# Performance work log

Hardware: AMD Instinct MI355X
Metric: run time of the kernel (lower is better)

## Reference

```python
import jax, jax.numpy as jnp
import numpy as np

BATCH, D_MODEL, D_STATE, L = 16, 512, 64, 4096
DT_MIN, DT_MAX = 1e-3, 0.1


def setup_inputs() -> dict:
    key = jax.random.key(0)
    ks = jax.random.split(key, 8)
    u = jax.random.normal(ks[0], (BATCH, D_MODEL, L), jnp.float32)
    # S4DKernel params (faithful init)
    log_dt = (jax.random.uniform(ks[1], (D_MODEL,), jnp.float32)
              * (np.log(DT_MAX) - np.log(DT_MIN)) + np.log(DT_MIN)).astype(jnp.float32)
    log_A_real = jnp.log(0.5 * jnp.ones((D_MODEL, D_STATE), jnp.float32))
    A_imag = jnp.pi * jnp.tile(jnp.arange(D_STATE, dtype=jnp.float32), (D_MODEL, 1))
    B_re = jnp.ones((D_MODEL, D_STATE), jnp.float32)
    B_im = jnp.zeros((D_MODEL, D_STATE), jnp.float32)
    # torch.randn(cfloat): re/im each N(0, 1/2)
    C_re = (2.0 ** -0.5) * jax.random.normal(ks[2], (D_MODEL, D_STATE), jnp.float32)
    C_im = (2.0 ** -0.5) * jax.random.normal(ks[3], (D_MODEL, D_STATE), jnp.float32)
    D = jax.random.normal(ks[4], (D_MODEL,), jnp.float32)
    # Conv1d(d_model, 2*d_model, k=1) weight squeezed to (2d, d)
    W_out = jax.random.normal(ks[5], (2 * D_MODEL, D_MODEL), jnp.float32) / np.sqrt(D_MODEL)
    b_out = jnp.zeros((2 * D_MODEL,), jnp.float32)
    # decoder Linear(d_model, 1)
    W_dec = jax.random.normal(ks[6], (1, D_MODEL), jnp.float32) / np.sqrt(D_MODEL)
    b_dec = jnp.zeros((1,), jnp.float32)
    return dict(u=u, log_dt=log_dt, log_A_real=log_A_real, A_imag=A_imag,
                B_re=B_re, B_im=B_im, C_re=C_re, C_im=C_im, D=D,
                W_out=W_out, b_out=b_out, W_dec=W_dec, b_dec=b_dec)


def _s4d_kernel(log_dt, log_A_real, A_imag, B_re, B_im, C_re, C_im, length):
    # ZOH discretization of diagonal SSM -> real conv kernel (d_model, length)
    dt = jnp.exp(log_dt)                                  # (d,)
    A = -jnp.exp(log_A_real) + 1j * A_imag                # (d, n)
    dtA = A * dt[:, None]                                 # (d, n)
    A_bar = jnp.exp(dtA)
    B = B_re + 1j * B_im
    C = C_re + 1j * C_im
    B_bar = (A_bar - 1.0) / A * B                         # (d, n)
    t = jnp.arange(length)
    # A_bar ** t == exp(dtA * t): (d, n, length) complex Vandermonde
    vand = jnp.exp(dtA[:, :, None] * t)
    K = jnp.einsum('dn,dnl->dl', C * B_bar, vand)         # sum over states
    return K.real


def reference(u, log_dt, log_A_real, A_imag, B_re, B_im, C_re, C_im, D,
              W_out, b_out, W_dec, b_dec):
    length = u.shape[-1]
    d_model = u.shape[1]
    K = _s4d_kernel(log_dt, log_A_real, A_imag, B_re, B_im, C_re, C_im, length)
    # depthwise causal conv: torch conv1d(padding=L-1, groups=d)[..., :L]
    y = jax.lax.conv_general_dilated(
        u, K[:, None, :], window_strides=(1,), padding=[(length - 1, 0)],
        feature_group_count=d_model, dimension_numbers=('NCH', 'OIH', 'NCH'))
    y = y + u * D[:, None]
    y = jax.nn.gelu(y, approximate=False)                 # exact GELU (erf)
    # 1x1 conv: d -> 2d
    y = jnp.einsum('oc,bcl->bol', W_out, y) + b_out[None, :, None]
    a, g = jnp.split(y, 2, axis=-2)                       # GLU on channel dim
    y = a * jax.nn.sigmoid(g)
    pooled = y.mean(axis=-1)                              # (B, d)
    return pooled @ W_dec.T + b_dec                       # (B, 1)
```

## Files before the change

### kernel.cpp

```cpp
#include <hip/hip_runtime.h>


#define UOFF_POOLED 1048576
#define UOFF_WBF    1081344
#define UOFF_UBF    2129920
#define UOFF_YRAW   69238784
#define UOFF_SEEDB  136347648
#define UOFF_KBUF   153124864

typedef __attribute__((ext_vector_type(8))) short short8;
typedef __attribute__((ext_vector_type(4))) float f32x4;
typedef __attribute__((ext_vector_type(2))) float f2;
typedef unsigned short ushort_t;
typedef unsigned int uint_t;

__device__ __forceinline__ ushort_t f2bf(float f) {
  uint_t u = __float_as_uint(f);
  u = (u + 0x7FFF + ((u >> 16) & 1)) >> 16;
  return (ushort_t)u;
}
__device__ __forceinline__ float bf2f(ushort_t v) {
  return __uint_as_float(((uint_t)v) << 16);
}

__device__ __forceinline__ void gload16(const ushort_t* g, ushort_t* l) {
  __builtin_amdgcn_global_load_lds(
      (const __attribute__((address_space(1))) void*)g,
      (__attribute__((address_space(3))) void*)l, 16, 0, 0);
}

__device__ __forceinline__ f2 cexp(float dr, float di, float t) {
  float e = expf(dr * t);
  float ph = di * t;
  return (f2){e * cosf(ph), e * sinf(ph)};
}

__global__ __launch_bounds__(256) void k_prep(
    const float* __restrict__ u, ushort_t* __restrict__ u_bf,
    const float* __restrict__ W_out, ushort_t* __restrict__ wbf,
    const float* __restrict__ log_dt, const float* __restrict__ log_A_real,
    const float* __restrict__ A_imag,
    const float* __restrict__ B_re, const float* __restrict__ B_im,
    const float* __restrict__ C_re, const float* __restrict__ C_im,
    float* __restrict__ p_ar, float* __restrict__ p_ai,
    float* __restrict__ p_wr, float* __restrict__ p_wi,
    float* __restrict__ p_dr, float* __restrict__ p_di,
    float* __restrict__ p_lr, float* __restrict__ p_li) {
  int bid = blockIdx.x;
  if (bid < 16384) {
    size_t i = (size_t)bid * 256 + threadIdx.x;
    const float4* p = (const float4*)u + 2 * i;
    float4 a = p[0], b = p[1];
    uint4 v;
    v.x = (uint_t)f2bf(a.x) | ((uint_t)f2bf(a.y) << 16);
    v.y = (uint_t)f2bf(a.z) | ((uint_t)f2bf(a.w) << 16);
    v.z = (uint_t)f2bf(b.x) | ((uint_t)f2bf(b.y) << 16);
    v.w = (uint_t)f2bf(b.z) | ((uint_t)f2bf(b.w) << 16);
    ((uint4*)u_bf)[i] = v;
  } else if (bid < 16384 + 2048) {
    int i = (bid - 16384) * 256 + threadIdx.x;
    if (i < 1024 * 512) wbf[i] = f2bf(W_out[i]);
  } else {
    int i = (bid - 18432) * 256 + threadIdx.x;
    int d = i >> 6;
    float dt  = expf(log_dt[d]);
    float Are = -expf(log_A_real[i]);
    float Aim = A_imag[i];
    float dre = dt * Are, dim = dt * Aim;
    float em  = expf(dre);
    float abr = em * cosf(dim);
    float abi = em * sinf(dim);
    float nr = abr - 1.0f, ni = abi;
    float inv = 1.0f / (Are * Are + Aim * Aim);
    float br = (nr * Are + ni * Aim) * inv;
    float bi = (ni * Are - nr * Aim) * inv;
    float Br = B_re[i], Bi = B_im[i];
    float b2r = br * Br - bi * Bi;
    float b2i = br * Bi + bi * Br;
    float Cr = C_re[i], Ci = C_im[i];
    p_ar[i] = abr; p_ai[i] = abi;
    p_wr[i] = Cr * b2r - Ci * b2i;
    p_wi[i] = Cr * b2i + Ci * b2r;
    p_dr[i] = dre; p_di[i] = dim;
    float eL = expf(dre * 4096.0f);
    float phL = dim * 4096.0f;
    p_lr[i] = eL * cosf(phL);
    p_li[i] = eL * sinf(phL);
  }
}

__global__ __launch_bounds__(256) void k_hk(
    const ushort_t* __restrict__ u_bf,
    const float* __restrict__ p_ar, const float* __restrict__ p_ai,
    const float* __restrict__ p_wr, const float* __restrict__ p_wi,
    const float* __restrict__ p_dr, const float* __restrict__ p_di,
    const float* __restrict__ Dvec,
    float2* __restrict__ Hbuf, ushort_t* __restrict__ Kbuf) {
  __shared__ ushort_t VLD[2][128][128];
  int bid = blockIdx.x;
  int d = bid >> 1;
  int tid = threadIdx.x;

  if (bid & 1) {
    int lane = tid & 63;
    int x0 = (tid >> 6) * 128;
    int i = d * 64 + lane;
    float ar = p_ar[i], ai = p_ai[i];
    float wr = p_wr[i], wi = p_wi[i];
    float Dd = Dvec[d];
    f2 e = cexp(p_dr[i], p_di[i], (float)(3584 + x0));
    float zr = wr * e.x - wi * e.y;
    float zi = wr * e.y + wi * e.x;
    for (int bb = 0; bb < 8; ++bb) {
      float s[16];
#pragma unroll
      for (int j = 0; j < 16; ++j) {
        s[j] = zr;
        float tr = zr * ar - zi * ai;
        zi = zr * ai + zi * ar;
        zr = tr;
      }
      float out = 0.f;
#pragma unroll
      for (int j = 0; j < 16; ++j) {
        float r = s[j];
#pragma unroll
        for (int off = 1; off < 64; off <<= 1) r += __shfl_xor(r, off, 64);
        if (lane == j) out = r;
      }
      if (lane < 16) {
        int x = x0 + bb * 16 + lane;
        Kbuf[d * 512 + x] = f2bf(x == 511 ? out + Dd : out);
      }
    }
    return;
  }

  int wv = tid >> 6, lane = tid & 63;
  int wm = wv >> 1, wn = wv & 1;
  int lrow = lane & 15, quad = lane >> 4;

  int m = tid & 127, chalf = tid >> 7;
  int nn = m >> 1, pp = m & 1;
  float ar = p_ar[d * 64 + nn], ai = p_ai[d * 64 + nn];
  float dr = p_dr[d * 64 + nn], di = p_di[d * 64 + nn];

  f32x4 acc[4][4];
#pragma unroll
  for (int mt = 0; mt < 4; ++mt)
#pragma unroll
    for (int nt = 0; nt < 4; ++nt) acc[mt][nt] = (f32x4){0.f, 0.f, 0.f, 0.f};

  auto gen = [&](int kt, int bs) {
    f2 z = cexp(dr, di, (float)(kt * 128 + chalf * 64));
#pragma unroll
    for (int g8 = 0; g8 < 8; ++g8) {
      ushort_t vals[8];
#pragma unroll
      for (int e = 0; e < 8; ++e) {
        vals[e] = f2bf(pp ? z.y : z.x);
        float zr = z.x * ar - z.y * ai;
        z.y = z.x * ai + z.y * ar;
        z.x = zr;
      }
      int g = (chalf * 64 + g8 * 8) >> 3;
      int gph = g ^ (m & 7);
      uint4 pk;
      pk.x = (uint_t)vals[0] | ((uint_t)vals[1] << 16);
      pk.y = (uint_t)vals[2] | ((uint_t)vals[3] << 16);
      pk.z = (uint_t)vals[4] | ((uint_t)vals[5] << 16);
      pk.w = (uint_t)vals[6] | ((uint_t)vals[7] << 16);
      *(uint4*)&VLD[bs][m][gph << 3] = pk;
    }
  };

  gen(0, 0);
  __syncthreads();
  for (int kt = 0; kt < 4; ++kt) {
    int cur = kt & 1;
    if (kt < 3) gen(kt + 1, cur ^ 1);
#pragma unroll
    for (int kb = 0; kb < 4; ++kb) {
      int kbase = kb * 32 + quad * 8;
      short8 af[4], bf[4];
#pragma unroll
      for (int mt = 0; mt < 4; ++mt) {
        int mrow = wm * 64 + mt * 16 + lrow;
        int gph = (kbase >> 3) ^ (mrow & 7);
        af[mt] = *(const short8*)&VLD[cur][mrow][gph << 3];
      }
#pragma unroll
      for (int nt = 0; nt < 4; ++nt) {
        int col = wn * 64 + nt * 16 + lrow;
        int b = col >> 3, c = col & 7;
        bf[nt] = *(const short8*)(u_bf + (size_t)(b * 512 + d) * 4096 + c * 512 + kt * 128 + kbase);
      }
#pragma unroll
      for (int mt = 0; mt < 4; ++mt)
#pragma unroll
        for (int nt = 0; nt < 4; ++nt)
          acc[mt][nt] = __builtin_amdgcn_mfma_f32_16x16x32_bf16(af[mt], bf[nt], acc[mt][nt], 0, 0, 0);
    }
    __syncthreads();
  }
#pragma unroll
  for (int mt = 0; mt < 4; ++mt) {
#pragma unroll
    for (int nt = 0; nt < 4; ++nt) {
      int col = wn * 64 + nt * 16 + lrow;
      int b = col >> 3, c = col & 7;
      int m0 = wm * 64 + mt * 16 + quad * 4;
      int n0 = m0 >> 1;
      float4 v = {acc[mt][nt][0], acc[mt][nt][1], acc[mt][nt][2], acc[mt][nt][3]};
      *(float4*)((float*)(Hbuf + ((size_t)((b * 8 + c) * 512 + d)) * 64 + n0)) = v;
    }
  }
}

__global__ __launch_bounds__(256) void k_seedpack(
    const float* __restrict__ p_dr, const float* __restrict__ p_di,
    const float2* __restrict__ Hbuf, ushort_t* __restrict__ seedB) {
  __shared__ ushort_t tile[128 * 128];
  int d = blockIdx.x;
  int tid = threadIdx.x;
  int n = tid >> 2;
  int bq = tid & 3;
  float dr = p_dr[d * 64 + n], di = p_di[d * 64 + n];
  f2 AS = cexp(dr, di, 512.0f);
  f2 R[8];
  R[0] = (f2){1.f, 0.f};
#pragma unroll
  for (int c = 1; c < 8; ++c)
    R[c] = (f2){R[c-1].x * AS.x - R[c-1].y * AS.y, R[c-1].x * AS.y + R[c-1].y * AS.x};
  for (int bb = 0; bb < 4; ++bb) {
    int b = bq * 4 + bb;
    f2 G = {0.f, 0.f};
#pragma unroll
    for (int c = 0; c < 8; ++c) {
      f2 T = R[7 - c];
      float sr = T.x * G.x - T.y * G.y;
      float si = T.x * G.y + T.y * G.x;
      int col = b * 8 + c;
      tile[col * 128 + 2 * n]     = f2bf(sr);
      tile[col * 128 + 2 * n + 1] = f2bf(si);
      float2 h = Hbuf[((size_t)((b * 8 + c) * 512 + d)) * 64 + n];
      G.x += R[c].x * h.x - R[c].y * h.y;
      G.y += R[c].x * h.y + R[c].y * h.x;
    }
  }
  __syncthreads();
  const uint4* src = (const uint4*)tile;
  uint4* dst = (uint4*)(seedB + (size_t)d * 16384);
  for (int k = tid; k < 2048; k += 256) dst[k] = src[k];
}

#define KRN 1048
__global__ __launch_bounds__(256) void k_conv(
    const ushort_t* __restrict__ u_bf, const ushort_t* __restrict__ Kbuf,
    const ushort_t* __restrict__ seedB,
    const float* __restrict__ p_ar, const float* __restrict__ p_ai,
    const float* __restrict__ p_wr, const float* __restrict__ p_wi,
    const float* __restrict__ p_dr, const float* __restrict__ p_di,
    ushort_t* __restrict__ yraw) {
  __shared__ ushort_t KRc[8][KRN];
  __shared__ ushort_t PLD[128][136];
  int id = blockIdx.x;
  int d = ((id >> 5) << 3) | (id & 7);
  int t0 = ((id >> 3) & 3) * 128;
  int tid = threadIdx.x;

  for (int e = tid; e < 8 * KRN; e += 256) {
    int r = e / KRN, x = e - r * KRN;
    int y = x + r;
    KRc[r][x] = (y < 512) ? Kbuf[d * 512 + y] : (ushort_t)0;
  }
  {
    int n = tid & 63, mh = tid >> 6;
    int i = d * 64 + n;
    float ar = p_ar[i], ai = p_ai[i];
    float wr = p_wr[i], wi = p_wi[i];
    int mtop = mh * 32 + 31;
    f2 E = cexp(p_dr[i], p_di[i], (float)(511 - t0 - mtop));
    float zr = wr * E.x - wi * E.y;
    float zi = wr * E.y + wi * E.x;
    for (int m = mtop; m >= mh * 32; --m) {
      PLD[m][2 * n]     = f2bf(zr);
      PLD[m][2 * n + 1] = f2bf(-zi);
      float tr = zr * ar - zi * ai;
      zi = zr * ai + zi * ar;
      zr = tr;
    }
  }
  __syncthreads();

  int wv = tid >> 6, lane = tid & 63;
  int wm = wv >> 1, wn = wv & 1;
  int lrow = lane & 15, quad = lane >> 4;
  f32x4 acc[4][4];
#pragma unroll
  for (int mt = 0; mt < 4; ++mt)
#pragma unroll
    for (int nt = 0; nt < 4; ++nt) acc[mt][nt] = (f32x4){0.f, 0.f, 0.f, 0.f};

  for (int kt = 0; kt < 16; ++kt) {
    int kbase = kt * 32 + quad * 8;
    short8 af[4], bf[4];
#pragma unroll
    for (int mt = 0; mt < 4; ++mt) {
      int mr = wm * 64 + mt * 16 + lrow;
      int idx = 511 - t0 - mr + kbase;
      int r = idx & 7, st = idx - r;
      af[mt] = *(const short8*)&KRc[r][st];
    }
#pragma unroll
    for (int nt = 0; nt < 4; ++nt) {
      int col = wn * 64 + nt * 16 + lrow;
      int b = col >> 3, c = col & 7;
      bf[nt] = *(const short8*)(u_bf + (size_t)(b * 512 + d) * 4096 + c * 512 + kbase);
    }
#pragma unroll
    for (int mt = 0; mt < 4; ++mt)
#pragma unroll
      for (int nt = 0; nt < 4; ++nt)
        acc[mt][nt] = __builtin_amdgcn_mfma_f32_16x16x32_bf16(af[mt], bf[nt], acc[mt][nt], 0, 0, 0);
  }
  for (int kt = 0; kt < 4; ++kt) {
    int k2 = kt * 32 + quad * 8;
    short8 af[4], bf[4];
#pragma unroll
    for (int mt = 0; mt < 4; ++mt)
      af[mt] = *(const short8*)&PLD[wm * 64 + mt * 16 + lrow][k2];
#pragma unroll
    for (int nt = 0; nt < 4; ++nt) {
      int col = wn * 64 + nt * 16 + lrow;
      bf[nt] = *(const short8*)(seedB + (size_t)d * 16384 + col * 128 + k2);
    }
#pragma unroll
    for (int mt = 0; mt < 4; ++mt)
#pragma unroll
      for (int nt = 0; nt < 4; ++nt)
        acc[mt][nt] = __builtin_amdgcn_mfma_f32_16x16x32_bf16(af[mt], bf[nt], acc[mt][nt], 0, 0, 0);
  }

#pragma unroll
  for (int mt = 0; mt < 4; ++mt) {
#pragma unroll
    for (int nt = 0; nt < 4; ++nt) {
      int col = wn * 64 + nt * 16 + lrow;
      int b = col >> 3, c = col & 7;
      int tau = t0 + wm * 64 + mt * 16 + quad * 4;
      uint_t lo = (uint_t)f2bf(acc[mt][nt][0]) | ((uint_t)f2bf(acc[mt][nt][1]) << 16);
      uint_t hi = (uint_t)f2bf(acc[mt][nt][2]) | ((uint_t)f2bf(acc[mt][nt][3]) << 16);
      uint2 vv = {lo, hi};
      *(uint2*)(yraw + (size_t)d * 65536 + b * 4096 + c * 512 + tau) = vv;
    }
  }
}

__global__ __launch_bounds__(256) void k_tg(
    const ushort_t* __restrict__ yraw, ushort_t* __restrict__ yg) {
  __shared__ ushort_t tile[64][72];
  int blk = blockIdx.x;
  int b = blk >> 9, dg = (blk >> 6) & 7, lg = blk & 63;
  int d0 = dg * 64, l0 = lg * 64;
  int tid = threadIdx.x;
  int dd = tid >> 2, lc = (tid & 3) * 16;

  const ushort_t* yp = yraw + (size_t)(d0 + dd) * 65536 + b * 4096 + l0 + lc;
  uint4 A0 = *(const uint4*)yp;
  uint4 A1 = *(const uint4*)(yp + 8);
  uint_t w[8] = {A0.x, A0.y, A0.z, A0.w, A1.x, A1.y, A1.z, A1.w};
#pragma unroll
  for (int i2 = 0; i2 < 16; ++i2) {
    ushort_t bits = (i2 & 1) ? (ushort_t)(w[i2 >> 1] >> 16) : (ushort_t)(w[i2 >> 1] & 0xffff);
    float y = bf2f(bits);
    float g = 0.5f * y * (1.0f + erff(y * 0.70710678118654752f));
    int row = lc + i2;
    int col = (dd + ((row >> 3) & 7) * 8) & 63;
    tile[row][col] = f2bf(g);
  }
  __syncthreads();
  int lr = tid >> 2, dc = (tid & 3) * 16;
  int rot = ((lr >> 3) & 7) * 8;
  int o1 = (dc + rot) & 63;
  int o2 = (dc + 8 + rot) & 63;
  uint4 v1 = *(const uint4*)&tile[lr][o1];
  uint4 v2 = *(const uint4*)&tile[lr][o2];
  ushort_t* og = yg + (size_t)b * (4096 * 512) + (size_t)(l0 + lr) * 512 + d0 + dc;
  *(uint4*)og = v1;
  *(uint4*)(og + 8) = v2;
}

__global__ __launch_bounds__(256) void k_gemm(
    const ushort_t* __restrict__ wbf, const ushort_t* __restrict__ yg,
    const float* __restrict__ b_out, float* __restrict__ pooled) {
  __shared__ ushort_t lwa[64][64];
  __shared__ ushort_t lwg[64][64];
  __shared__ ushort_t ly[128][64];
  int tid = threadIdx.x;
  int id = blockIdx.x;
  int p = id >> 8, m = (id >> 5) & 7, q = id & 31;
  int mp0 = m * 64;
  int n0 = (p * 32 + q) * 128;
  int b = n0 >> 12;
  int wv = tid >> 6, lane = tid & 63;
  int mh = wv >> 1, nh = wv & 1;
  int lrow = lane & 15, quad = lane >> 4;
  f32x4 accA[2][4], accG[2][4];
#pragma unroll
  for (int mt = 0; mt < 2; ++mt)
#pragma unroll
    for (int nt = 0; nt < 4; ++nt) {
      accA[mt][nt] = (f32x4){0.f, 0.f, 0.f, 0.f};
      accG[mt][nt] = (f32x4){0.f, 0.f, 0.f, 0.f};
    }

  int sub = lane >> 3;
  int gsw = ((lane & 7) ^ (sub & 7)) * 8;
  const ushort_t* gA0 = wbf + (size_t)(mp0 + wv * 16 + sub) * 512 + gsw;
  const ushort_t* gA1 = gA0 + 8 * 512;
  const ushort_t* gG0 = gA0 + (size_t)512 * 512;
  const ushort_t* gG1 = gA1 + (size_t)512 * 512;
  const ushort_t* gY0 = yg + (size_t)(n0 + wv * 32 + sub) * 512 + gsw;
  const ushort_t* gY1 = gY0 + 8 * 512;
  const ushort_t* gY2 = gY0 + 16 * 512;
  const ushort_t* gY3 = gY0 + 24 * 512;
  ushort_t* lA0 = &lwa[wv * 16][0];
  ushort_t* lA1 = &lwa[wv * 16 + 8][0];
  ushort_t* lG0 = &lwg[wv * 16][0];
  ushort_t* lG1 = &lwg[wv * 16 + 8][0];
  ushort_t* lY0 = &ly[wv * 32][0];
  ushort_t* lY1 = &ly[wv * 32 + 8][0];
  ushort_t* lY2 = &ly[wv * 32 + 16][0];
  ushort_t* lY3 = &ly[wv * 32 + 24][0];

  for (int kc = 0; kc < 8; ++kc) {
    int off = kc * 64;
    gload16(gA0 + off, lA0);
    gload16(gA1 + off, lA1);
    gload16(gG0 + off, lG0);
    gload16(gG1 + off, lG1);
    gload16(gY0 + off, lY0);
    gload16(gY1 + off, lY1);
    gload16(gY2 + off, lY2);
    gload16(gY3 + off, lY3);
    __syncthreads();
#pragma unroll
    for (int kb = 0; kb < 2; ++kb) {
      int kg = kb * 4 + quad;
      short8 bfv[4], af[2], gf[2];
#pragma unroll
      for (int nt = 0; nt < 4; ++nt) {
        int row = nh * 64 + nt * 16 + lrow;
        bfv[nt] = *(const short8*)&ly[row][(kg ^ (row & 7)) << 3];
      }
#pragma unroll
      for (int mt = 0; mt < 2; ++mt) {
        int row = mh * 32 + mt * 16 + lrow;
        af[mt] = *(const short8*)&lwa[row][(kg ^ (row & 7)) << 3];
        gf[mt] = *(const short8*)&lwg[row][(kg ^ (row & 7)) << 3];
      }
#pragma unroll
      for (int mt = 0; mt < 2; ++mt)
#pragma unroll
        for (int nt = 0; nt < 4; ++nt) {
          accA[mt][nt] = __builtin_amdgcn_mfma_f32_16x16x32_bf16(af[mt], bfv[nt], accA[mt][nt], 0, 0, 0);
          accG[mt][nt] = __builtin_amdgcn_mfma_f32_16x16x32_bf16(gf[mt], bfv[nt], accG[mt][nt], 0, 0, 0);
        }
    }
    __syncthreads();
  }
#pragma unroll
  for (int mt = 0; mt < 2; ++mt) {
#pragma unroll
    for (int reg = 0; reg < 4; ++reg) {
      int olocal = mh * 32 + mt * 16 + quad * 4 + reg;
      float ba = b_out[mp0 + olocal];
      float bg = b_out[512 + mp0 + olocal];
      float h = 0.f;
#pragma unroll
      for (int nt = 0; nt < 4; ++nt) {
        float a = accA[mt][nt][reg] + ba;
        float gv = accG[mt][nt][reg] + bg;
        h += a / (1.0f + __expf(-gv));
      }
#pragma unroll
      for (int off = 1; off < 16; off <<= 1) h += __shfl_xor(h, off, 16);
      if (lrow == 0) atomicAdd(&pooled[b * 512 + mp0 + olocal], h);
    }
  }
}

__global__ void k_final(const float* __restrict__ pooled, const float* __restrict__ W_dec,
                        const float* __restrict__ b_dec, float* __restrict__ out) {
  int b = blockIdx.x;
  int lane = threadIdx.x;
  float s = 0.f;
#pragma unroll
  for (int j = 0; j < 8; ++j) s += pooled[b * 512 + lane + 64 * j] * W_dec[lane + 64 * j];
#pragma unroll
  for (int off = 1; off < 64; off <<= 1) s += __shfl_xor(s, off, 64);
  if (lane == 0) out[b] = s * (1.0f / 4096.0f) + b_dec[0];
}

extern "C" void kernel_launch(void* const* d_in, const int* in_sizes, int n_in,
                              void* d_out, int out_size, void* d_ws, size_t ws_size,
                              hipStream_t stream) {
  const float* u          = (const float*)d_in[0];
  const float* log_dt     = (const float*)d_in[1];
  const float* log_A_real = (const float*)d_in[2];
  const float* A_imag     = (const float*)d_in[3];
  const float* B_re       = (const float*)d_in[4];
  const float* B_im       = (const float*)d_in[5];
  const float* C_re       = (const float*)d_in[6];
  const float* C_im       = (const float*)d_in[7];
  const float* Dv         = (const float*)d_in[8];
  const float* W_out      = (const float*)d_in[9];
  const float* b_out      = (const float*)d_in[10];
  const float* W_dec      = (const float*)d_in[11];
  const float* b_dec      = (const float*)d_in[12];

  float* ws = (float*)d_ws;
  float* p_ar = ws;
  float* p_ai = ws + 32768;
  float* p_wr = ws + 65536;
  float* p_wi = ws + 98304;
  float* p_dr = ws + 131072;
  float* p_di = ws + 163840;
  float* p_lr = ws + 196608;
  float* p_li = ws + 229376;
  float* pooled = (float*)((char*)d_ws + UOFF_POOLED);
  ushort_t* wbf   = (ushort_t*)((char*)d_ws + UOFF_WBF);
  ushort_t* u_bf  = (ushort_t*)((char*)d_ws + UOFF_UBF);
  ushort_t* yg    = (ushort_t*)((char*)d_ws + UOFF_UBF);
  ushort_t* yraw  = (ushort_t*)((char*)d_ws + UOFF_YRAW);
  float2*   Hbuf  = (float2*)((char*)d_ws + UOFF_YRAW);
  ushort_t* seedB = (ushort_t*)((char*)d_ws + UOFF_SEEDB);
  ushort_t* Kbuf  = (ushort_t*)((char*)d_ws + UOFF_KBUF);

  hipMemsetAsync(pooled, 0, 16 * 512 * sizeof(float), stream);
  k_prep<<<18560, 256, 0, stream>>>(u, u_bf, W_out, wbf,
                                    log_dt, log_A_real, A_imag, B_re, B_im, C_re, C_im,
                                    p_ar, p_ai, p_wr, p_wi, p_dr, p_di, p_lr, p_li);
  k_hk<<<1024, 256, 0, stream>>>(u_bf, p_ar, p_ai, p_wr, p_wi, p_dr, p_di, Dv,
                                 Hbuf, Kbuf);
  k_seedpack<<<512, 256, 0, stream>>>(p_dr, p_di, Hbuf, seedB);
  k_conv<<<2048, 256, 0, stream>>>(u_bf, Kbuf, seedB,
                                   p_ar, p_ai, p_wr, p_wi, p_dr, p_di, yraw);
  k_tg<<<8192, 256, 0, stream>>>(yraw, yg);
  k_gemm<<<4096, 256, 0, stream>>>(wbf, yg, b_out, pooled);
  k_final<<<16, 64, 0, stream>>>(pooled, W_dec, b_dec, (float*)d_out);
}
```

Before: 497.0 us.

## Fuse seed-pack stage into k_hk via shared memory, restructure K load loop

The chunk-state accumulation and bf16 seed packing from k_seedpack now run at the tail of k_hk. The per-chunk H values are staged in shared memory (reusing the VLD buffer) instead of being written to a global Hbuf and read back by a separate launch. This drops one kernel launch and the global round trip of H. The KRc fill loop in k_conv is also restructured to avoid an integer division per element. The fused tail adds shared-memory traffic and a sync to the k_hk blocks that take the MFMA path.

After: 489.3 us. No clear change (-1.6%).

```diff
diff --git a/kernel.cpp b/kernel.cpp
--- a/kernel.cpp
+++ b/kernel.cpp
@@ -95,7 +95,7 @@
     const float* __restrict__ p_wr, const float* __restrict__ p_wi,
     const float* __restrict__ p_dr, const float* __restrict__ p_di,
     const float* __restrict__ Dvec,
-    float2* __restrict__ Hbuf, ushort_t* __restrict__ Kbuf) {
+    ushort_t* __restrict__ seedB, ushort_t* __restrict__ Kbuf) {
   __shared__ ushort_t VLD[2][128][128];
   int bid = blockIdx.x;
   int d = bid >> 1;
@@ -203,55 +203,55 @@
     }
     __syncthreads();
   }
+
+  float2* Hl = (float2*)VLD;
+  ushort_t* tile = (ushort_t*)VLD + 16384;
 #pragma unroll
   for (int mt = 0; mt < 4; ++mt) {
 #pragma unroll
     for (int nt = 0; nt < 4; ++nt) {
       int col = wn * 64 + nt * 16 + lrow;
-      int b = col >> 3, c = col & 7;
       int m0 = wm * 64 + mt * 16 + quad * 4;
       int n0 = m0 >> 1;
       float4 v = {acc[mt][nt][0], acc[mt][nt][1], acc[mt][nt][2], acc[mt][nt][3]};
-      *(float4*)((float*)(Hbuf + ((size_t)((b * 8 + c) * 512 + d)) * 64 + n0)) = v;
-    }
-  }
-}
-
-__global__ __launch_bounds__(256) void k_seedpack(
-    const float* __restrict__ p_dr, const float* __restrict__ p_di,
-    const float2* __restrict__ Hbuf, ushort_t* __restrict__ seedB) {
-  __shared__ ushort_t tile[128 * 128];
-  int d = blockIdx.x;
-  int tid = threadIdx.x;
-  int n = tid >> 2;
-  int bq = tid & 3;
-  float dr = p_dr[d * 64 + n], di = p_di[d * 64 + n];
-  f2 AS = cexp(dr, di, 512.0f);
-  f2 R[8];
-  R[0] = (f2){1.f, 0.f};
-#pragma unroll
-  for (int c = 1; c < 8; ++c)
-    R[c] = (f2){R[c-1].x * AS.x - R[c-1].y * AS.y, R[c-1].x * AS.y + R[c-1].y * AS.x};
-  for (int bb = 0; bb < 4; ++bb) {
-    int b = bq * 4 + bb;
-    f2 G = {0.f, 0.f};
-#pragma unroll
-    for (int c = 0; c < 8; ++c) {
-      f2 T = R[7 - c];
-      float sr = T.x * G.x - T.y * G.y;
-      float si = T.x * G.y + T.y * G.x;
-      int col = b * 8 + c;
-      tile[col * 128 + 2 * n]     = f2bf(sr);
-      tile[col * 128 + 2 * n + 1] = f2bf(si);
-      float2 h = Hbuf[((size_t)((b * 8 + c) * 512 + d)) * 64 + n];
-      G.x += R[c].x * h.x - R[c].y * h.y;
-      G.y += R[c].x * h.y + R[c].y * h.x;
+      *(float4*)&Hl[col * 64 + n0] = v;
     }
   }
   __syncthreads();
-  const uint4* src = (const uint4*)tile;
-  uint4* dst = (uint4*)(seedB + (size_t)d * 16384);
-  for (int k = tid; k < 2048; k += 256) dst[k] = src[k];
+
+  {
+    int n = tid >> 2;
+    int bq = tid & 3;
+    float sdr = p_dr[d * 64 + n], sdi = p_di[d * 64 + n];
+    f2 AS = cexp(sdr, sdi, 512.0f);
+    f2 R[8];
+    R[0] = (f2){1.f, 0.f};
+#pragma unroll
+    for (int c = 1; c < 8; ++c)
+      R[c] = (f2){R[c-1].x * AS.x - R[c-1].y * AS.y, R[c-1].x * AS.y + R[c-1].y * AS.x};
+    for (int bb = 0; bb < 4; ++bb) {
+      int b = bq * 4 + bb;
+      f2 G = {0.f, 0.f};
+#pragma unroll
+      for (int c = 0; c < 8; ++c) {
+        f2 T = R[7 - c];
+        float sr = T.x * G.x - T.y * G.y;
+        float si = T.x * G.y + T.y * G.x;
+        int col = b * 8 + c;
+        tile[col * 128 + 2 * n]     = f2bf(sr);
+        tile[col * 128 + 2 * n + 1] = f2bf(si);
+        float2 h = Hl[(b * 8 + c) * 64 + n];
+        G.x += R[c].x * h.x - R[c].y * h.y;
+        G.y += R[c].x * h.y + R[c].y * h.x;
+      }
+    }
+  }
+  __syncthreads();
+  {
+    const uint4* src = (const uint4*)tile;
+    uint4* dst = (uint4*)(seedB + (size_t)d * 16384);
+    for (int k = tid; k < 2048; k += 256) dst[k] = src[k];
+  }
 }
 
 #define KRN 1048
@@ -269,11 +269,12 @@
   int t0 = ((id >> 3) & 3) * 128;
   int tid = threadIdx.x;
 
-  for (int e = tid; e < 8 * KRN; e += 256) {
-    int r = e / KRN, x = e - r * KRN;
-    int y = x + r;
-    KRc[r][x] = (y < 512) ? Kbuf[d * 512 + y] : (ushort_t)0;
-  }
+#pragma unroll
+  for (int r = 0; r < 8; ++r)
+    for (int x = tid; x < KRN; x += 256) {
+      int y = x + r;
+      KRc[r][x] = (y < 512) ? Kbuf[d * 512 + y] : (ushort_t)0;
+    }
   {
     int n = tid & 63, mh = tid >> 6;
     int i = d * 64 + n;
@@ -534,7 +535,6 @@
   ushort_t* u_bf  = (ushort_t*)((char*)d_ws + UOFF_UBF);
   ushort_t* yg    = (ushort_t*)((char*)d_ws + UOFF_UBF);
   ushort_t* yraw  = (ushort_t*)((char*)d_ws + UOFF_YRAW);
-  float2*   Hbuf  = (float2*)((char*)d_ws + UOFF_YRAW);
   ushort_t* seedB = (ushort_t*)((char*)d_ws + UOFF_SEEDB);
   ushort_t* Kbuf  = (ushort_t*)((char*)d_ws + UOFF_KBUF);
 
@@ -543,8 +543,7 @@
                                     log_dt, log_A_real, A_imag, B_re, B_im, C_re, C_im,
                                     p_ar, p_ai, p_wr, p_wi, p_dr, p_di, p_lr, p_li);
   k_hk<<<1024, 256, 0, stream>>>(u_bf, p_ar, p_ai, p_wr, p_wi, p_dr, p_di, Dv,
-                                 Hbuf, Kbuf);
-  k_seedpack<<<512, 256, 0, stream>>>(p_dr, p_di, Hbuf, seedB);
+                                 seedB, Kbuf);
   k_conv<<<2048, 256, 0, stream>>>(u_bf, Kbuf, seedB,
                                    p_ar, p_ai, p_wr, p_wi, p_dr, p_di, yraw);
   k_tg<<<8192, 256, 0, stream>>>(yraw, yg);
```
